# Kernel optimization log

Measured on AMD Instinct MI355X. Metric: run time of the kernel, lower is better.

Reference implementation:

```python
import jax, jax.numpy as jnp
import numpy as np

THETA = 10000.0
BLOCK_SIZE = 8192  # max_cache_len; T >= BLOCK_SIZE triggers eviction
NEG_INF = -1e30


def _rope_cos_sin(head_dim, seq_len, dtype):
    inv_freq = 1.0 / (THETA ** (jnp.arange(0, head_dim, 2, dtype=jnp.float32) / head_dim))
    freqs = jnp.arange(seq_len, dtype=jnp.float32)[:, None] * inv_freq[None, :]  # (T, hd/2)
    return jnp.cos(freqs).astype(dtype), jnp.sin(freqs).astype(dtype)


def _apply_rope(x, cos, sin):
    # x: (B, T, hd); complex multiply on interleaved pairs, matching torch.view_as_complex
    B, T, hd = x.shape
    xr = x.reshape(B, T, hd // 2, 2)
    x0, x1 = xr[..., 0], xr[..., 1]
    out = jnp.stack([x0 * cos - x1 * sin, x0 * sin + x1 * cos], axis=-1)
    return out.reshape(B, T, hd)


def setup_inputs() -> dict:
    key = jax.random.key(0)
    kx, kk, kq, kv = jax.random.split(key, 4)
    B, T, C, hd = 1, 8192, 1024, 64
    x = jax.random.normal(kx, (B, T, C), dtype=jnp.float32)
    Wk = 0.02 * jax.random.normal(kk, (C, hd), dtype=jnp.float32)
    Wq = 0.02 * jax.random.normal(kq, (C, hd), dtype=jnp.float32)
    Wv = 0.02 * jax.random.normal(kv, (C, hd), dtype=jnp.float32)
    return {"x": x, "Wk": Wk, "Wq": Wq, "Wv": Wv}


def reference(x, Wk, Wq, Wv):
    # Warm-up branch of Head.forward: RoPE QK causal attention + importance-based eviction.
    B, T, C = x.shape
    hd = Wk.shape[1]
    k = x @ Wk  # (B, T, hd)
    q = x @ Wq
    v = x @ Wv
    cos, sin = _rope_cos_sin(hd, T, x.dtype)
    k = _apply_rope(k, cos, sin)
    q = _apply_rope(q, cos, sin)
    scale = hd ** -0.5
    scores = jnp.einsum('btd,bsd->bts', q, k) * scale  # (B, T, T)
    causal = jnp.tril(jnp.ones((T, T), dtype=bool))
    scores = jnp.where(causal[None], scores, NEG_INF)
    wei = jax.nn.softmax(scores, axis=-1)
    out = jnp.einsum('bts,bsd->btd', wei, v)  # (B, T, hd)
    # importance-based KV-cache eviction (T >= BLOCK_SIZE here)
    col_sums = wei.sum(axis=1)  # (B, T)
    evict_id = jnp.argmin(col_sums.reshape(-1))  # flattened argmin, as torch.argmin (B=1)
    keep = jnp.arange(T - 1)
    keep = keep + (keep >= evict_id)  # all indices except evict_id
    importance = jnp.take(wei, keep, axis=1)  # evict row in dim 1: (B, T-1, T)
    cache_k = jnp.take(k, keep, axis=1)       # (B, T-1, hd)
    cache_v = jnp.take(v, keep, axis=1)       # (B, T-1, hd)
    return out, importance, cache_k, cache_v
```

## Files before the change

kernel.cpp:

```cpp
#include <hip/hip_runtime.h>

#define TT 8192
#define CC 1024
#define HD 64
#define TAIL0 (TT - 64)
#define IMP_OFF ((size_t)TT * HD)
#define CK_OFF (IMP_OFF + (size_t)(TT - 1) * TT)
#define CV_OFF (CK_OFF + (size_t)(TT - 1) * HD)

typedef float f32x4 __attribute__((ext_vector_type(4)));
typedef short short8 __attribute__((ext_vector_type(8)));

static __device__ __forceinline__ short f2bf(float f) {
  union { float f; unsigned u; } v; v.f = f;
  unsigned u = v.u;
  unsigned r = (u + 0x7fffu + ((u >> 16) & 1u)) >> 16;
  return (short)r;
}
static __device__ __forceinline__ float bf2f(short h) {
  union { unsigned u; float f; } v;
  v.u = ((unsigned)(unsigned short)h) << 16;
  return v.f;
}
static __device__ __forceinline__ f32x4 mfma16(short8 a, short8 b, f32x4 c) {
  return __builtin_amdgcn_mfma_f32_16x16x32_bf16(a, b, c, 0, 0, 0);
}
static __device__ __forceinline__ void nt_store4(float* p, f32x4 v) {
  __builtin_nontemporal_store(v, (f32x4*)p);
}

__global__ void prep(const float* __restrict__ Wk, const float* __restrict__ Wq,
                     const float* __restrict__ Wv, short* __restrict__ wth,
                     short* __restrict__ wtl, float* __restrict__ colsums,
                     float* __restrict__ ctab, float* __restrict__ stab) {
  const int b = blockIdx.x;
  if (b < 768) {
    const int tid = b * 256 + threadIdx.x;
    const int col = tid >> 10, c = tid & 1023;
    const int m = col >> 6, d = col & 63;
    const float* W = (m == 0) ? Wk : (m == 1) ? Wq : Wv;
    const float w = W[c * HD + d];
    const short h = f2bf(w);
    wth[col * CC + c] = h;
    wtl[col * CC + c] = f2bf(w - bf2f(h));
  } else if (b < 800) {
    const int t = (b - 768) * 256 + threadIdx.x;
    colsums[t] = 0.0f;
  } else {
    const int t = (b - 800) * 256 + threadIdx.x;
    const int row = t >> 5, fi = t & 31;
    const float inv = (float)(1.0 / pow(10000.0, (double)fi / 32.0));
    const float ang = (float)row * inv;
    float sn, cs;
    sincosf(ang, &sn, &cs);
    ctab[t] = cs; stab[t] = sn;
  }
}

__global__ __launch_bounds__(256) void qkv_rope(
    const float* __restrict__ x, const short* __restrict__ wth,
    const short* __restrict__ wtl, const float* __restrict__ ctab,
    const float* __restrict__ stab,
    short* __restrict__ qb, short* __restrict__ kbb, short* __restrict__ vbb,
    float* __restrict__ kf, float* __restrict__ vf, float* __restrict__ qf) {
  __shared__ short xsh[16][1024];
  __shared__ short xsl[16][1024];
  const int tid = threadIdx.x;
  const int lane = tid & 63, wv = tid >> 6;
  const int g = lane >> 4, lr = lane & 15, g8 = g * 8;
  const int r0 = blockIdx.x * 16;

  for (int i = tid; i < 16 * 128; i += 256) {
    const int row = i >> 7, u = i & 127;
    const float4 a4 = *(const float4*)&x[(size_t)(r0 + row) * CC + u * 8];
    const float4 b4 = *(const float4*)&x[(size_t)(r0 + row) * CC + u * 8 + 4];
    const float xv[8] = {a4.x, a4.y, a4.z, a4.w, b4.x, b4.y, b4.z, b4.w};
    short8 h, l;
#pragma unroll
    for (int t = 0; t < 8; ++t) {
      h[t] = f2bf(xv[t]);
      l[t] = f2bf(xv[t] - bf2f(h[t]));
    }
    const int us = (u ^ (row & 7)) * 8;
    *(short8*)&xsh[row][us] = h;
    *(short8*)&xsl[row][us] = l;
  }
  __syncthreads();

  const int ct0 = wv * 3;
  f32x4 acc[3];
#pragma unroll
  for (int i = 0; i < 3; ++i) acc[i] = (f32x4){0.f, 0.f, 0.f, 0.f};
  for (int kc = 0; kc < 32; ++kc) {
    const int us = ((kc * 4 + g) ^ (lr & 7)) * 8;
    const short8 ah = *(const short8*)&xsh[lr][us];
    const short8 al = *(const short8*)&xsl[lr][us];
    const int k0 = kc * 32 + g8;
#pragma unroll
    for (int t = 0; t < 3; ++t) {
      const int ct = ct0 + t;
      const short8 bh = *(const short8*)&wth[(ct * 16 + lr) * CC + k0];
      const short8 bl = *(const short8*)&wtl[(ct * 16 + lr) * CC + k0];
      acc[t] = mfma16(ah, bh, acc[t]);
      acc[t] = mfma16(al, bh, acc[t]);
      acc[t] = mfma16(ah, bl, acc[t]);
    }
  }
#pragma unroll
  for (int t = 0; t < 3; ++t) {
    const int col = ct0 * 16 + t * 16 + lr;
    const int m = col >> 6, d = col & 63;
#pragma unroll
    for (int r = 0; r < 4; ++r) {
      const int row = r0 + g * 4 + r;
      const float val = acc[t][r];
      if (m == 2) {
        vf[row * HD + d] = val;
        const int kp = row >> 5, r32 = row & 31;
        const int gv = r32 >> 3, tv = r32 & 7;
        const int ctv = d >> 4, lrv = d & 15;
        vbb[kp * 2048 + ctv * 512 + gv * 128 + lrv * 8 + tv] = f2bf(val);
      } else {
        const float partner = __shfl_xor(val, 1);
        const int fi = d >> 1;
        const float cs = ctab[row * 32 + fi];
        const float sn = stab[row * 32 + fi];
        const float res = (d & 1) ? (partner * sn + val * cs)
                                  : (val * cs - partner * sn);
        if (m == 0) {
          kf[row * HD + d] = res;
          const int kt = row >> 4, lrk = row & 15;
          const int hh = d >> 5, gk = (d & 31) >> 3, tk = d & 7;
          kbb[kt * 1024 + hh * 512 + gk * 128 + lrk * 8 + tk] = f2bf(res);
        } else {
          qf[row * HD + d] = res;
          qb[row * HD + d] = f2bf(res);
        }
      }
    }
  }
}

__global__ __launch_bounds__(1024) void attn_row(
    const short* __restrict__ qb, const short* __restrict__ kbb,
    const short* __restrict__ vbb, float* __restrict__ colsums,
    float* __restrict__ outp, float* __restrict__ stash,
    float* __restrict__ linv_g) {
  const int tid = threadIdx.x;
  const int lane = tid & 63, wv = tid >> 6;
  const int g = lane >> 4, lr = lane & 15, g8 = g * 8;
  const int bid = (int)blockIdx.x;
  const int rt = (bid < 256) ? (511 - bid) : (bid - 256);
  const int r0 = rt * 16, rmax = r0 + 15;
  const int nkt = rt + 1;
  const int nktp = (nkt + 1) >> 1;
  float* imp = outp + IMP_OFF;
  const f32x4 z4 = (f32x4){0.f, 0.f, 0.f, 0.f};

  __shared__ float et[16][16][36];
  __shared__ float l4[16][16];

  const short8 a0 = *(const short8*)&qb[(r0 + lr) * HD + g8];
  const short8 a1 = *(const short8*)&qb[(r0 + lr) * HD + 32 + g8];
  const int ln8 = lane * 8;

  float lacc[4] = {0.f, 0.f, 0.f, 0.f};
  for (int kt = wv; kt < nkt; kt += 16) {
    const short8 b0 = *(const short8*)&kbb[kt * 1024 + ln8];
    const short8 b1 = *(const short8*)&kbb[kt * 1024 + 512 + ln8];
    f32x4 sv = z4;
    sv = mfma16(a0, b0, sv);
    sv = mfma16(a1, b1, sv);
    const int j = kt * 16 + lr;
#pragma unroll
    for (int r = 0; r < 4; ++r) {
      const int i = r0 + g * 4 + r;
      if (j <= i) lacc[r] += __expf(sv[r] * 0.125f);
    }
  }
#pragma unroll
  for (int r = 0; r < 4; ++r) {
#pragma unroll
    for (int m = 1; m < 16; m <<= 1) lacc[r] += __shfl_xor(lacc[r], m);
  }
  if (lr == 0) {
#pragma unroll
    for (int r = 0; r < 4; ++r) l4[wv][g * 4 + r] = lacc[r];
  }
  __syncthreads();
  float rinv[4];
#pragma unroll
  for (int r = 0; r < 4; ++r) {
    const int row = g * 4 + r;
    float s = 0.f;
#pragma unroll
    for (int w = 0; w < 16; ++w) s += l4[w][row];
    rinv[r] = 1.0f / s;
  }
  if (wv == 0 && lr == 0) {
#pragma unroll
    for (int r = 0; r < 4; ++r) linv_g[r0 + g * 4 + r] = rinv[r];
  }

  f32x4 oacc[4];
#pragma unroll
  for (int ct = 0; ct < 4; ++ct) oacc[ct] = z4;
  const int worow = lane >> 3, wof4 = (lane & 7) * 4;
  for (int kp = wv; kp < nktp; kp += 16) {
    const int j0p = kp * 32;
    short8 bv[4];
#pragma unroll
    for (int ct = 0; ct < 4; ++ct)
      bv[ct] = *(const short8*)&vbb[kp * 2048 + ct * 512 + ln8];
#pragma unroll
    for (int h = 0; h < 2; ++h) {
      const int kt = kp * 2 + h;
      const int j0 = j0p + h * 16;
      float w4[4] = {0.f, 0.f, 0.f, 0.f};
      if (j0 <= rmax) {
        const short8 b0 = *(const short8*)&kbb[kt * 1024 + ln8];
        const short8 b1 = *(const short8*)&kbb[kt * 1024 + 512 + ln8];
        f32x4 sv = z4;
        sv = mfma16(a0, b0, sv);
        sv = mfma16(a1, b1, sv);
        const int j = j0 + lr;
#pragma unroll
        for (int r = 0; r < 4; ++r) {
          const int i = r0 + g * 4 + r;
          w4[r] = (j <= i) ? __expf(sv[r] * 0.125f) * rinv[r] : 0.0f;
        }
        float csum = w4[0] + w4[1] + w4[2] + w4[3];
        csum += __shfl_xor(csum, 16);
        csum += __shfl_xor(csum, 32);
        if (lane < 16 && csum > 0.f) atomicAdd(&colsums[j0 + lane], csum);
      }
#pragma unroll
      for (int r = 0; r < 4; ++r) et[wv][g * 4 + r][h * 16 + lr] = w4[r];
    }
    const float4 e0 = *(const float4*)&et[wv][lr][g8];
    const float4 e1 = *(const float4*)&et[wv][lr][g8 + 4];
    short8 ea;
    ea[0] = f2bf(e0.x); ea[1] = f2bf(e0.y); ea[2] = f2bf(e0.z); ea[3] = f2bf(e0.w);
    ea[4] = f2bf(e1.x); ea[5] = f2bf(e1.y); ea[6] = f2bf(e1.z); ea[7] = f2bf(e1.w);
#pragma unroll
    for (int ct = 0; ct < 4; ++ct) oacc[ct] = mfma16(ea, bv[ct], oacc[ct]);
#pragma unroll
    for (int p = 0; p < 2; ++p) {
      const int row = p * 8 + worow;
      const int i = r0 + row;
      const f32x4 v = *(const f32x4*)&et[wv][row][wof4];
      if (i < TT - 1) nt_store4(&imp[(size_t)i * TT + j0p + wof4], v);
      else            *(f32x4*)&stash[j0p + wof4] = v;
    }
  }
  const int zstart = nktp * 32;
  for (int row = 0; row < 16; ++row) {
    const int i = r0 + row;
    if (i < TT - 1) {
      float* dst = &imp[(size_t)i * TT];
      for (int c = zstart + tid * 4; c < TT; c += 4096) nt_store4(&dst[c], z4);
    } else {
      for (int c = zstart + tid * 4; c < TT; c += 4096) *(f32x4*)&stash[c] = z4;
    }
  }
  __syncthreads();
  float* cbuf = &et[0][0][0];
#pragma unroll
  for (int step = 8; step >= 1; step >>= 1) {
    if (wv >= step && wv < 2 * step) {
      float* dst = cbuf + (size_t)(wv - step) * 1024;
#pragma unroll
      for (int ct = 0; ct < 4; ++ct)
#pragma unroll
        for (int r = 0; r < 4; ++r)
          dst[(g * 4 + r) * 64 + ct * 16 + lr] = oacc[ct][r];
    }
    __syncthreads();
    if (wv < step) {
      const float* src = cbuf + (size_t)wv * 1024;
#pragma unroll
      for (int ct = 0; ct < 4; ++ct)
#pragma unroll
        for (int r = 0; r < 4; ++r)
          oacc[ct][r] += src[(g * 4 + r) * 64 + ct * 16 + lr];
    }
    __syncthreads();
  }
  if (wv == 0) {
#pragma unroll
    for (int ct = 0; ct < 4; ++ct)
#pragma unroll
      for (int r = 0; r < 4; ++r)
        outp[(size_t)(r0 + g * 4 + r) * HD + ct * 16 + lr] = oacc[ct][r];
  }
}

__global__ __launch_bounds__(256) void tail_exact(
    const float* __restrict__ qf, const float* __restrict__ kf,
    float* __restrict__ l_exact, float* __restrict__ tail_e) {
  const int b = blockIdx.x;
  const int i = TAIL0 + b;
  const int tid = threadIdx.x;
  __shared__ float qs[64];
  __shared__ float ws4[4];
  if (tid < 64) {
    qs[tid] = qf[i * HD + tid];
    if (TAIL0 + tid > i) tail_e[(b << 6) + tid] = 0.0f;
  }
  __syncthreads();
  float part = 0.f;
  for (int j = tid; j <= i; j += 256) {
    const float* kr = &kf[(size_t)j * HD];
    float dot = 0.f;
#pragma unroll
    for (int d = 0; d < 64; ++d) dot += qs[d] * kr[d];
    const float e = expf(dot * 0.125f);
    part += e;
    if (j >= TAIL0) tail_e[(b << 6) + (j - TAIL0)] = e;
  }
#pragma unroll
  for (int m = 1; m < 64; m <<= 1) part += __shfl_xor(part, m);
  if ((tid & 63) == 0) ws4[tid >> 6] = part;
  __syncthreads();
  if (tid == 0) l_exact[b] = ws4[0] + ws4[1] + ws4[2] + ws4[3];
}

__global__ void argmin_k(const float* __restrict__ colsums,
                         const float* __restrict__ l_exact,
                         const float* __restrict__ tail_e,
                         int* __restrict__ evict) {
  __shared__ float sv[4];
  __shared__ int si[4];
  const int tid = threadIdx.x, lane = tid & 63, wv = tid >> 6;
  float best = 3.4e38f; int bi = TT;
  for (int j = tid; j < TT; j += 256) {
    float v;
    if (j >= TAIL0) {
      const int jc = j - TAIL0;
      v = 0.f;
      for (int b = jc; b < 64; ++b) v += tail_e[(b << 6) + jc] / l_exact[b];
    } else {
      v = colsums[j];
    }
    if (v < best) { best = v; bi = j; }
  }
#pragma unroll
  for (int m = 1; m < 64; m <<= 1) {
    const float ov = __shfl_xor(best, m);
    const int oi = __shfl_xor(bi, m);
    if (ov < best || (ov == best && oi < bi)) { best = ov; bi = oi; }
  }
  if (lane == 0) { sv[wv] = best; si[wv] = bi; }
  __syncthreads();
  if (tid == 0) {
    for (int w = 1; w < 4; ++w)
      if (sv[w] < best || (sv[w] == best && si[w] < bi)) { best = sv[w]; bi = si[w]; }
    evict[0] = bi;
  }
}

__global__ __launch_bounds__(256) void fix_cache(
    const float* __restrict__ qf, const float* __restrict__ kf,
    const float* __restrict__ vf, const float* __restrict__ linv,
    const float* __restrict__ stash, const int* __restrict__ evict,
    float* __restrict__ outp) {
  const int bid = (int)blockIdx.x;
  const int tid = threadIdx.x;
  const int eid = evict[0];
  if (bid < 512) {
    float* imp = outp + IMP_OFF;
    __shared__ float qs[64];
    for (int dst = eid + bid; dst < TT - 1; dst += 512) {
      const int src = dst + 1;
      if (src == TT - 1) {
        for (int c = tid; c < TT / 4; c += 256)
          ((f32x4*)&imp[(size_t)dst * TT])[c] = ((const f32x4*)stash)[c];
      } else {
        if (tid < 64) qs[tid] = qf[src * HD + tid];
        __syncthreads();
        const float rinv = linv[src];
        for (int j = tid; j < TT; j += 256) {
          float w = 0.f;
          if (j <= src) {
            const float* kr = &kf[(size_t)j * HD];
            float dot = 0.f;
#pragma unroll
            for (int d = 0; d < 64; ++d) dot += qs[d] * kr[d];
            w = expf(dot * 0.125f) * rinv;
          }
          imp[(size_t)dst * TT + j] = w;
        }
        __syncthreads();
      }
    }
  } else {
    const int t = (bid - 512) * 256 + tid;
    const int per = (TT - 1) * (HD / 4);
    if (t >= 2 * per) return;
    const int m = t / per;
    const int rem = t - m * per;
    const int r = rem >> 4, c4 = rem & 15;
    const int src = r + (r >= eid);
    const float* sp = m ? vf : kf;
    const f32x4 val = *(const f32x4*)&sp[src * HD + c4 * 4];
    float* dst = outp + (m ? CV_OFF : CK_OFF);
    nt_store4(&dst[r * HD + c4 * 4], val);
  }
}

extern "C" void kernel_launch(void* const* d_in, const int* in_sizes, int n_in,
                              void* d_out, int out_size, void* d_ws, size_t ws_size,
                              hipStream_t stream) {
  const float* x  = (const float*)d_in[0];
  const float* Wk = (const float*)d_in[1];
  const float* Wq = (const float*)d_in[2];
  const float* Wv = (const float*)d_in[3];
  float* outp = (float*)d_out;
  char* ws = (char*)d_ws;
  short* qb      = (short*)(ws);
  short* kbb     = (short*)(ws + (1u << 20));
  short* vbb     = (short*)(ws + (2u << 20));
  float* kf      = (float*)(ws + (3u << 20));
  float* vf      = (float*)(ws + (5u << 20));
  float* qf      = (float*)(ws + (7u << 20));
  float* linv    = (float*)(ws + (9u << 20));
  int*   evict   = (int*)  (ws + (9u << 20) + (64u << 10));
  float* colsums = (float*)(ws + (9u << 20) + (384u << 10));
  short* wth     = (short*)(ws + (9u << 20) + (448u << 10));
  short* wtl     = (short*)(ws + (9u << 20) + (832u << 10));
  float* tail_e  = (float*)(ws + (9u << 20) + (1280u << 10));
  float* l_exact = (float*)(ws + (9u << 20) + (1344u << 10));
  float* stash   = (float*)(ws + (9u << 20) + (1408u << 10));
  float* ctab    = (float*)(ws + (12u << 20));
  float* stab    = (float*)(ws + (13u << 20));

  prep<<<1824, 256, 0, stream>>>(Wk, Wq, Wv, wth, wtl, colsums, ctab, stab);
  qkv_rope<<<512, 256, 0, stream>>>(x, wth, wtl, ctab, stab, qb, kbb, vbb, kf, vf, qf);
  attn_row<<<512, 1024, 0, stream>>>(qb, kbb, vbb, colsums, outp, stash, linv);
  tail_exact<<<64, 256, 0, stream>>>(qf, kf, l_exact, tail_e);
  argmin_k<<<1, 256, 0, stream>>>(colsums, l_exact, tail_e, evict);
  fix_cache<<<1536, 256, 0, stream>>>(qf, kf, vf, linv, stash, evict, outp);
}
```

Measured before the change: 230.3 us.

## Replace column-sum atomics with per-row-tile partials plus reduce kernel; halve qkv LDS

Attention blocks now write per-row-tile column partial sums into a 512x8192 scratch buffer instead of issuing atomicAdd on the shared colsums array. A separate reduction kernel then sums those partials per column. This removes atomic contention on colsums, at the cost of about 16 MB of extra writes and reads plus one more kernel launch. Separately, the QKV projection stages x through shared memory in two 512-wide halves, halving the LDS footprint to allow higher occupancy, but it adds an extra barrier per half.

```diff
diff --git a/kernel.cpp b/kernel.cpp
--- a/kernel.cpp
+++ b/kernel.cpp
@@ -31,8 +31,8 @@
 
 __global__ void prep(const float* __restrict__ Wk, const float* __restrict__ Wq,
                      const float* __restrict__ Wv, short* __restrict__ wth,
-                     short* __restrict__ wtl, float* __restrict__ colsums,
-                     float* __restrict__ ctab, float* __restrict__ stab) {
+                     short* __restrict__ wtl, float* __restrict__ ctab,
+                     float* __restrict__ stab) {
   const int b = blockIdx.x;
   if (b < 768) {
     const int tid = b * 256 + threadIdx.x;
@@ -43,11 +43,8 @@
     const short h = f2bf(w);
     wth[col * CC + c] = h;
     wtl[col * CC + c] = f2bf(w - bf2f(h));
-  } else if (b < 800) {
+  } else {
     const int t = (b - 768) * 256 + threadIdx.x;
-    colsums[t] = 0.0f;
-  } else {
-    const int t = (b - 800) * 256 + threadIdx.x;
     const int row = t >> 5, fi = t & 31;
     const float inv = (float)(1.0 / pow(10000.0, (double)fi / 32.0));
     const float ang = (float)row * inv;
@@ -63,48 +60,52 @@
     const float* __restrict__ stab,
     short* __restrict__ qb, short* __restrict__ kbb, short* __restrict__ vbb,
     float* __restrict__ kf, float* __restrict__ vf, float* __restrict__ qf) {
-  __shared__ short xsh[16][1024];
-  __shared__ short xsl[16][1024];
+  __shared__ short xsh[16][512];
+  __shared__ short xsl[16][512];
   const int tid = threadIdx.x;
   const int lane = tid & 63, wv = tid >> 6;
   const int g = lane >> 4, lr = lane & 15, g8 = g * 8;
   const int r0 = blockIdx.x * 16;
 
-  for (int i = tid; i < 16 * 128; i += 256) {
-    const int row = i >> 7, u = i & 127;
-    const float4 a4 = *(const float4*)&x[(size_t)(r0 + row) * CC + u * 8];
-    const float4 b4 = *(const float4*)&x[(size_t)(r0 + row) * CC + u * 8 + 4];
-    const float xv[8] = {a4.x, a4.y, a4.z, a4.w, b4.x, b4.y, b4.z, b4.w};
-    short8 h, l;
-#pragma unroll
-    for (int t = 0; t < 8; ++t) {
-      h[t] = f2bf(xv[t]);
-      l[t] = f2bf(xv[t] - bf2f(h[t]));
-    }
-    const int us = (u ^ (row & 7)) * 8;
-    *(short8*)&xsh[row][us] = h;
-    *(short8*)&xsl[row][us] = l;
-  }
-  __syncthreads();
-
   const int ct0 = wv * 3;
   f32x4 acc[3];
 #pragma unroll
   for (int i = 0; i < 3; ++i) acc[i] = (f32x4){0.f, 0.f, 0.f, 0.f};
-  for (int kc = 0; kc < 32; ++kc) {
-    const int us = ((kc * 4 + g) ^ (lr & 7)) * 8;
-    const short8 ah = *(const short8*)&xsh[lr][us];
-    const short8 al = *(const short8*)&xsl[lr][us];
-    const int k0 = kc * 32 + g8;
-#pragma unroll
-    for (int t = 0; t < 3; ++t) {
-      const int ct = ct0 + t;
-      const short8 bh = *(const short8*)&wth[(ct * 16 + lr) * CC + k0];
-      const short8 bl = *(const short8*)&wtl[(ct * 16 + lr) * CC + k0];
-      acc[t] = mfma16(ah, bh, acc[t]);
-      acc[t] = mfma16(al, bh, acc[t]);
-      acc[t] = mfma16(ah, bl, acc[t]);
-    }
+
+  for (int half = 0; half < 2; ++half) {
+    const int cbase = half * 512;
+    for (int i = tid; i < 16 * 64; i += 256) {
+      const int row = i >> 6, u = i & 63;
+      const float4 a4 = *(const float4*)&x[(size_t)(r0 + row) * CC + cbase + u * 8];
+      const float4 b4 = *(const float4*)&x[(size_t)(r0 + row) * CC + cbase + u * 8 + 4];
+      const float xv[8] = {a4.x, a4.y, a4.z, a4.w, b4.x, b4.y, b4.z, b4.w};
+      short8 h, l;
+#pragma unroll
+      for (int t = 0; t < 8; ++t) {
+        h[t] = f2bf(xv[t]);
+        l[t] = f2bf(xv[t] - bf2f(h[t]));
+      }
+      const int us = (u ^ (row & 7)) * 8;
+      *(short8*)&xsh[row][us] = h;
+      *(short8*)&xsl[row][us] = l;
+    }
+    __syncthreads();
+    for (int kc = 0; kc < 16; ++kc) {
+      const int us = ((kc * 4 + g) ^ (lr & 7)) * 8;
+      const short8 ah = *(const short8*)&xsh[lr][us];
+      const short8 al = *(const short8*)&xsl[lr][us];
+      const int k0 = cbase + kc * 32 + g8;
+#pragma unroll
+      for (int t = 0; t < 3; ++t) {
+        const int ct = ct0 + t;
+        const short8 bh = *(const short8*)&wth[(ct * 16 + lr) * CC + k0];
+        const short8 bl = *(const short8*)&wtl[(ct * 16 + lr) * CC + k0];
+        acc[t] = mfma16(ah, bh, acc[t]);
+        acc[t] = mfma16(al, bh, acc[t]);
+        acc[t] = mfma16(ah, bl, acc[t]);
+      }
+    }
+    __syncthreads();
   }
 #pragma unroll
   for (int t = 0; t < 3; ++t) {
@@ -143,7 +144,7 @@
 
 __global__ __launch_bounds__(1024) void attn_row(
     const short* __restrict__ qb, const short* __restrict__ kbb,
-    const short* __restrict__ vbb, float* __restrict__ colsums,
+    const short* __restrict__ vbb, float* __restrict__ colp,
     float* __restrict__ outp, float* __restrict__ stash,
     float* __restrict__ linv_g) {
   const int tid = threadIdx.x;
@@ -155,6 +156,7 @@
   const int nkt = rt + 1;
   const int nktp = (nkt + 1) >> 1;
   float* imp = outp + IMP_OFF;
+  float* cp = colp + (size_t)rt * TT;
   const f32x4 z4 = (f32x4){0.f, 0.f, 0.f, 0.f};
 
   __shared__ float et[16][16][36];
@@ -232,7 +234,7 @@
         float csum = w4[0] + w4[1] + w4[2] + w4[3];
         csum += __shfl_xor(csum, 16);
         csum += __shfl_xor(csum, 32);
-        if (lane < 16 && csum > 0.f) atomicAdd(&colsums[j0 + lane], csum);
+        if (lane < 16) cp[j0 + lane] = csum;
       }
 #pragma unroll
       for (int r = 0; r < 4; ++r) et[wv][g * 4 + r][h * 16 + lr] = w4[r];
@@ -263,6 +265,7 @@
       for (int c = zstart + tid * 4; c < TT; c += 4096) *(f32x4*)&stash[c] = z4;
     }
   }
+  for (int c = nkt * 16 + tid; c < TT; c += 1024) cp[c] = 0.0f;
   __syncthreads();
   float* cbuf = &et[0][0][0];
 #pragma unroll
@@ -293,6 +296,14 @@
       for (int r = 0; r < 4; ++r)
         outp[(size_t)(r0 + g * 4 + r) * HD + ct * 16 + lr] = oacc[ct][r];
   }
+}
+
+__global__ void colsum_reduce(const float* __restrict__ colp,
+                              float* __restrict__ colsums) {
+  const int j = blockIdx.x * 256 + threadIdx.x;
+  float s = 0.f;
+  for (int rt = 0; rt < 512; ++rt) s += colp[(size_t)rt * TT + j];
+  colsums[j] = s;
 }
 
 __global__ __launch_bounds__(256) void tail_exact(
@@ -433,10 +444,12 @@
   float* stash   = (float*)(ws + (9u << 20) + (1408u << 10));
   float* ctab    = (float*)(ws + (12u << 20));
   float* stab    = (float*)(ws + (13u << 20));
-
-  prep<<<1824, 256, 0, stream>>>(Wk, Wq, Wv, wth, wtl, colsums, ctab, stab);
+  float* colp    = (float*)(ws + (16u << 20));
+
+  prep<<<1792, 256, 0, stream>>>(Wk, Wq, Wv, wth, wtl, ctab, stab);
   qkv_rope<<<512, 256, 0, stream>>>(x, wth, wtl, ctab, stab, qb, kbb, vbb, kf, vf, qf);
-  attn_row<<<512, 1024, 0, stream>>>(qb, kbb, vbb, colsums, outp, stash, linv);
+  attn_row<<<512, 1024, 0, stream>>>(qb, kbb, vbb, colp, outp, stash, linv);
+  colsum_reduce<<<32, 256, 0, stream>>>(colp, colsums);
   tail_exact<<<64, 256, 0, stream>>>(qf, kf, l_exact, tail_e);
   argmin_k<<<1, 256, 0, stream>>>(colsums, l_exact, tail_e, evict);
   fix_cache<<<1536, 256, 0, stream>>>(qf, kf, vf, linv, stash, evict, outp);
```

After: 244.1 us. 6.0% more time.
